# Optimization experiments

Measured on AMD Instinct MI355X. Metric: run time of the kernel, lower is better.

Reference implementation:

```python
import jax, jax.numpy as jnp
import numpy as np

B, S, D, H = 2, 2048, 1024, 16
HD = D // H  # head_size = 64


def setup_inputs() -> dict:
    key = jax.random.key(0)
    ks = jax.random.split(key, 11)
    s = 1.0 / np.sqrt(D)
    inp = {
        "q": jax.random.normal(ks[0], (B, S, D), jnp.float32),
        "k": jax.random.normal(ks[1], (B, S, D), jnp.float32),
        "v": jax.random.normal(ks[2], (B, S, D), jnp.float32),
        "Wq": jax.random.normal(ks[3], (D, D), jnp.float32) * s,
        "bq": jax.random.normal(ks[4], (D,), jnp.float32) * s,
        "Wk": jax.random.normal(ks[5], (D, D), jnp.float32) * s,
        "bk": jax.random.normal(ks[6], (D,), jnp.float32) * s,
        "Wv": jax.random.normal(ks[7], (D, D), jnp.float32) * s,
        "bv": jax.random.normal(ks[8], (D,), jnp.float32) * s,
        "Wo": jax.random.normal(ks[9], (D, D), jnp.float32) * s,
        "bo": jax.random.normal(ks[10], (D,), jnp.float32) * s,
    }
    return inp


def reference(q, k, v, Wq, bq, Wk, bk, Wv, bv, Wo, bo):
    # project and split heads: [B,S,D] -> [B,H,S,HD]
    def split_heads(x, W, b):
        y = x @ W.T + b
        return y.reshape(B, S, H, HD).transpose(0, 2, 1, 3)

    qh = split_heads(q, Wq, bq)
    kh = split_heads(k, Wk, bk)
    vh = split_heads(v, Wv, bv)

    scale = 1.0 / jnp.sqrt(jnp.asarray(HD, qh.dtype))
    scores = jnp.einsum("bhqd,bhkd->bhqk", qh, kh) * scale  # [B,H,S,S]
    weights = jax.nn.softmax(scores, axis=-1)
    out = jnp.einsum("bhqk,bhkd->bhqd", weights, vh)  # [B,H,S,HD]
    out = out.transpose(0, 2, 1, 3).reshape(B, S, D)
    return out @ Wo.T + bo
```

## Files before the change

kernel.cpp:

```cpp
#include <hip/hip_runtime.h>

typedef __attribute__((ext_vector_type(4))) float f32x4;
typedef __attribute__((ext_vector_type(8))) short bf16x8;
typedef __attribute__((ext_vector_type(8))) unsigned short u16x8;
typedef __attribute__((ext_vector_type(4))) unsigned short u16x4;
typedef __attribute__((ext_vector_type(4))) unsigned int u32x4;
typedef unsigned short ushort_t;

#define LOG2E 1.4426950408889634f

__device__ inline unsigned short f2bf(float x) {
  union { float f; unsigned int u; } v; v.f = x;
  unsigned int r = v.u + 0x7fffu + ((v.u >> 16) & 1u);
  return (unsigned short)(r >> 16);
}

__device__ inline unsigned cvtpk_bf16(float a, float b) {
  unsigned r;
  asm("v_cvt_pk_bf16_f32 %0, %1, %2" : "=v"(r) : "v"(a), "v"(b));
  return r;
}

__device__ inline void gload_lds16(const void* g, void* l) {
  __builtin_amdgcn_global_load_lds(
      (const __attribute__((address_space(1))) unsigned int*)g,
      (__attribute__((address_space(3))) unsigned int*)l, 16, 0, 0);
}

__device__ inline void cvt_body(const float* __restrict__ src, ushort_t* __restrict__ dst, int i) {
  const f32x4* s = (const f32x4*)src;
  f32x4 a = s[2 * i], b = s[2 * i + 1];
  u16x8 o;
#pragma unroll
  for (int j = 0; j < 4; ++j) { o[j] = f2bf(a[j]); o[4 + j] = f2bf(b[j]); }
  *(u16x8*)(dst + (size_t)i * 8) = o;
}

__global__ __launch_bounds__(256) void cvt_bf16(const float* __restrict__ src,
                                                ushort_t* __restrict__ dst, int n8) {
  int i = blockIdx.x * 256 + threadIdx.x;
  if (i < n8) cvt_body(src, dst, i);
}

__global__ __launch_bounds__(256) void cvt3(const float* __restrict__ a,
                                            const float* __restrict__ b,
                                            const float* __restrict__ c,
                                            ushort_t* __restrict__ dst, int n8) {
  int i = blockIdx.x * 256 + threadIdx.x;
  if (i >= n8) return;
  const float* s = blockIdx.y == 0 ? a : (blockIdx.y == 1 ? b : c);
  cvt_body(s, dst + (size_t)blockIdx.y * n8 * 8, i);
}

__global__ __launch_bounds__(256) void cvt4(const float* __restrict__ a,
                                            const float* __restrict__ b,
                                            const float* __restrict__ c,
                                            const float* __restrict__ d,
                                            ushort_t* __restrict__ dst, int n8) {
  int i = blockIdx.x * 256 + threadIdx.x;
  if (i >= n8) return;
  const float* s = blockIdx.y == 0 ? a : (blockIdx.y == 1 ? b : (blockIdx.y == 2 ? c : d));
  cvt_body(s, dst + (size_t)blockIdx.y * n8 * 8, i);
}

template <typename F>
__device__ inline void gemm_core(const ushort_t* __restrict__ A, const ushort_t* __restrict__ W,
                                 int m0, int n0, ushort_t* As, ushort_t* Bs, F&& mfma_step) {
  constexpr int K = 1024;
  const int tid = threadIdx.x, lane = tid & 63, wid = tid >> 6;
  const int srow = lane >> 2, sp = lane & 3;
  for (int k0 = 0; k0 < K; k0 += 32) {
#pragma unroll
    for (int c = 0; c < 2; ++c) {
      int i = wid * 2 + c;
      int row = i * 16 + srow;
      int s = sp ^ ((row >> 1) & 3);
      gload_lds16(A + (size_t)(m0 + row) * K + k0 + s * 8, &As[i * 512]);
      gload_lds16(W + (size_t)(n0 + row) * K + k0 + s * 8, &Bs[i * 512]);
    }
    __syncthreads();
    mfma_step(As, Bs);
    __syncthreads();
  }
}

__global__ __launch_bounds__(256) void proj_gemm(const ushort_t* __restrict__ Abase, int aStride,
                                                 const ushort_t* __restrict__ Wall, int wStride,
                                                 const float* __restrict__ bq,
                                                 const float* __restrict__ bk,
                                                 const float* __restrict__ bv, float qs,
                                                 ushort_t* __restrict__ outQ,
                                                 ushort_t* __restrict__ outK,
                                                 ushort_t* __restrict__ outV, int zofs) {
  __shared__ __attribute__((aligned(16))) ushort_t As[128 * 32];
  __shared__ __attribute__((aligned(16))) ushort_t Bs[128 * 32];
  const int z = blockIdx.z + zofs;
  const ushort_t* A = Abase + (size_t)z * aStride;
  const ushort_t* W = Wall + (size_t)z * wStride;
  const float* bias = z == 0 ? bq : (z == 1 ? bk : bv);
  const float scale = z == 0 ? qs : 1.0f;
  ushort_t* out = z == 0 ? outQ : (z == 1 ? outK : outV);
  const int mode = z == 2 ? 1 : 0;

  const int tid = threadIdx.x, lane = tid & 63, wid = tid >> 6;
  const int m0 = blockIdx.x * 128, n0 = blockIdx.y * 128;
  const int wm = wid >> 1, wn = wid & 1;
  const int qr = lane & 15, kq = lane >> 4;
  f32x4 acc[4][4] = {};

  gemm_core(A, W, m0, n0, As, Bs, [&](ushort_t* as, ushort_t* bs) {
    bf16x8 a[4], b[4];
#pragma unroll
    for (int f = 0; f < 4; ++f) {
      int ra = wm * 64 + f * 16 + qr;
      a[f] = *(const bf16x8*)&as[ra * 32 + (kq ^ ((ra >> 1) & 3)) * 8];
      int rb = wn * 64 + f * 16 + qr;
      b[f] = *(const bf16x8*)&bs[rb * 32 + (kq ^ ((rb >> 1) & 3)) * 8];
    }
#pragma unroll
    for (int i = 0; i < 4; ++i)
#pragma unroll
      for (int j = 0; j < 4; ++j)
        acc[i][j] = __builtin_amdgcn_mfma_f32_16x16x32_bf16(a[i], b[j], acc[i][j], 0, 0, 0);
  });

  const int cm = m0 + wm * 64, cn = n0 + wn * 64;
#pragma unroll
  for (int fn = 0; fn < 4; ++fn) {
    int n = cn + fn * 16 + qr;
    float bvv = bias[n];
    int h = n >> 6, hd = n & 63;
#pragma unroll
    for (int fm = 0; fm < 4; ++fm) {
      int m = cm + fm * 16 + kq * 4;
      if (mode == 0) {
#pragma unroll
        for (int r = 0; r < 4; ++r) {
          int mm = m + r, b = mm >> 11, s = mm & 2047;
          out[((size_t)(b * 16 + h) * 2048 + s) * 64 + hd] = f2bf((acc[fm][fn][r] + bvv) * scale);
        }
      } else {
        int b = m >> 11, s = m & 2047;
        u16x4 pk;
#pragma unroll
        for (int r = 0; r < 4; ++r) pk[r] = f2bf((acc[fm][fn][r] + bvv) * scale);
        *(u16x4*)&out[((size_t)(b * 16 + h) * 64 + hd) * 2048 + s] = pk;
      }
    }
  }
}

__global__ __launch_bounds__(256) void gemm_out(const ushort_t* __restrict__ A,
                                                const ushort_t* __restrict__ W,
                                                const float* __restrict__ bias,
                                                float* __restrict__ out) {
  __shared__ __attribute__((aligned(16))) ushort_t As[128 * 32];
  __shared__ __attribute__((aligned(16))) ushort_t Bs[128 * 32];
  const int tid = threadIdx.x, lane = tid & 63, wid = tid >> 6;
  const int m0 = blockIdx.x * 128, n0 = blockIdx.y * 128;
  const int wm = wid >> 1, wn = wid & 1;
  const int qr = lane & 15, kq = lane >> 4;
  f32x4 acc[4][4] = {};

  gemm_core(A, W, m0, n0, As, Bs, [&](ushort_t* as, ushort_t* bs) {
    bf16x8 a[4], b[4];
#pragma unroll
    for (int f = 0; f < 4; ++f) {
      int ra = wm * 64 + f * 16 + qr;
      a[f] = *(const bf16x8*)&as[ra * 32 + (kq ^ ((ra >> 1) & 3)) * 8];
      int rb = wn * 64 + f * 16 + qr;
      b[f] = *(const bf16x8*)&bs[rb * 32 + (kq ^ ((rb >> 1) & 3)) * 8];
    }
#pragma unroll
    for (int i = 0; i < 4; ++i)
#pragma unroll
      for (int j = 0; j < 4; ++j)
        acc[i][j] = __builtin_amdgcn_mfma_f32_16x16x32_bf16(a[i], b[j], acc[i][j], 0, 0, 0);
  });

  const int cm = m0 + wm * 64, cn = n0 + wn * 64;
#pragma unroll
  for (int fn = 0; fn < 4; ++fn) {
    int n = cn + fn * 16 + qr;
    float bvv = bias[n];
#pragma unroll
    for (int fm = 0; fm < 4; ++fm) {
      int m = cm + fm * 16 + kq * 4;
#pragma unroll
      for (int r = 0; r < 4; ++r) out[(size_t)(m + r) * 1024 + n] = acc[fm][fn][r] + bvv;
    }
  }
}

__global__ __launch_bounds__(256) void attn_fwd(const ushort_t* __restrict__ Qh,
                                                const ushort_t* __restrict__ Kh,
                                                const ushort_t* __restrict__ Vt,
                                                ushort_t* __restrict__ ctx) {
  constexpr int S = 2048, HD = 64, NT = S / 64;
  __shared__ __attribute__((aligned(16))) ushort_t Ks[2][64 * 64];
  __shared__ __attribute__((aligned(16))) ushort_t Vs[2][64 * 64];

  const int tid = threadIdx.x, lane = tid & 63, wid = tid >> 6;
  const int bh = blockIdx.y, qt = blockIdx.x;
  const size_t head = (size_t)bh * S * HD;
  const ushort_t* Qp = Qh + head;
  const ushort_t* Kp = Kh + head;
  const ushort_t* Vp = Vt + head;

  const int qr = lane & 15, kq = lane >> 4;
  const int q0 = qt * 128 + wid * 32;

  bf16x8 qfA[2], qfB[2];
#pragma unroll
  for (int kh = 0; kh < 2; ++kh) {
    qfA[kh] = *(const bf16x8*)&Qp[(size_t)(q0 + qr) * HD + kh * 32 + kq * 8];
    qfB[kh] = *(const bf16x8*)&Qp[(size_t)(q0 + 16 + qr) * HD + kh * 32 + kq * 8];
  }

  f32x4 accA[4] = {}, accB[4] = {};
  float mrunA = -3e38f, lrunA = 0.f;
  float mrunB = -3e38f, lrunB = 0.f;

  const int srow8 = lane >> 3, sp8 = lane & 7;

  for (int t = 0; t < NT; ++t) {
    const int buf = t & 1;
    {
      int kv0 = t == 0 ? 0 : (t + 1) * 64;
      int dbuf = t == 0 ? 0 : buf ^ 1;
      if (t == 0 || t + 1 < NT) {
#pragma unroll
        for (int c = 0; c < 2; ++c) {
          int i = wid * 2 + c;
          int row = i * 8 + srow8;
          int s = sp8 ^ (row & 7);
          gload_lds16(&Kp[(size_t)(kv0 + row) * HD + s * 8], &Ks[dbuf][i * 512]);
          gload_lds16(&Vp[(size_t)row * S + kv0 + s * 8], &Vs[dbuf][i * 512]);
        }
      }
      if (t == 0) {
        __syncthreads();
        if (NT > 1) {
#pragma unroll
          for (int c = 0; c < 2; ++c) {
            int i = wid * 2 + c;
            int row = i * 8 + srow8;
            int s = sp8 ^ (row & 7);
            gload_lds16(&Kp[(size_t)(64 + row) * HD + s * 8], &Ks[1][i * 512]);
            gload_lds16(&Vp[(size_t)row * S + 64 + s * 8], &Vs[1][i * 512]);
          }
        }
      }
    }

    f32x4 scA[4] = {}, scB[4] = {};
    __builtin_amdgcn_s_setprio(1);
#pragma unroll
    for (int fn = 0; fn < 4; ++fn) {
      int rk = fn * 16 + qr;
#pragma unroll
      for (int kh = 0; kh < 2; ++kh) {
        bf16x8 kf = *(const bf16x8*)&Ks[buf][rk * 64 + (((kh * 4 + kq) ^ (rk & 7)) * 8)];
        scA[fn] = __builtin_amdgcn_mfma_f32_16x16x32_bf16(kf, qfA[kh], scA[fn], 0, 0, 0);
        scB[fn] = __builtin_amdgcn_mfma_f32_16x16x32_bf16(kf, qfB[kh], scB[fn], 0, 0, 0);
      }
    }
    __builtin_amdgcn_s_setprio(0);

    unsigned wvA[4][2], wvB[4][2];
    {
      float t0 = fmaxf(fmaxf(fmaxf(scA[0][0], scA[0][1]), scA[0][2]), scA[0][3]);
      float t1 = fmaxf(fmaxf(fmaxf(scA[1][0], scA[1][1]), scA[1][2]), scA[1][3]);
      float t2 = fmaxf(fmaxf(fmaxf(scA[2][0], scA[2][1]), scA[2][2]), scA[2][3]);
      float t3 = fmaxf(fmaxf(fmaxf(scA[3][0], scA[3][1]), scA[3][2]), scA[3][3]);
      float pm = fmaxf(fmaxf(t0, t1), fmaxf(t2, t3));
      pm = fmaxf(pm, __shfl_xor(pm, 16, 64));
      pm = fmaxf(pm, __shfl_xor(pm, 32, 64));
      bool need = pm > mrunA + 8.0f;
      if (__any(need)) {
        float mn = need ? pm : mrunA;
        float sf = __builtin_amdgcn_exp2f(mrunA - mn);
        mrunA = mn;
#pragma unroll
        for (int f2 = 0; f2 < 4; ++f2) accA[f2] *= sf;
        lrunA *= sf;
      }
      float sum = 0.f;
#pragma unroll
      for (int fn = 0; fn < 4; ++fn)
#pragma unroll
        for (int r = 0; r < 4; ++r) {
          float p = __builtin_amdgcn_exp2f(scA[fn][r] - mrunA);
          scA[fn][r] = p;
          sum += p;
        }
      sum += __shfl_xor(sum, 16, 64);
      sum += __shfl_xor(sum, 32, 64);
      lrunA += sum;
#pragma unroll
      for (int fn = 0; fn < 4; ++fn) {
        wvA[fn][0] = cvtpk_bf16(scA[fn][0], scA[fn][1]);
        wvA[fn][1] = cvtpk_bf16(scA[fn][2], scA[fn][3]);
      }
    }
    {
      float t0 = fmaxf(fmaxf(fmaxf(scB[0][0], scB[0][1]), scB[0][2]), scB[0][3]);
      float t1 = fmaxf(fmaxf(fmaxf(scB[1][0], scB[1][1]), scB[1][2]), scB[1][3]);
      float t2 = fmaxf(fmaxf(fmaxf(scB[2][0], scB[2][1]), scB[2][2]), scB[2][3]);
      float t3 = fmaxf(fmaxf(fmaxf(scB[3][0], scB[3][1]), scB[3][2]), scB[3][3]);
      float pm = fmaxf(fmaxf(t0, t1), fmaxf(t2, t3));
      pm = fmaxf(pm, __shfl_xor(pm, 16, 64));
      pm = fmaxf(pm, __shfl_xor(pm, 32, 64));
      bool need = pm > mrunB + 8.0f;
      if (__any(need)) {
        float mn = need ? pm : mrunB;
        float sf = __builtin_amdgcn_exp2f(mrunB - mn);
        mrunB = mn;
#pragma unroll
        for (int f2 = 0; f2 < 4; ++f2) accB[f2] *= sf;
        lrunB *= sf;
      }
      float sum = 0.f;
#pragma unroll
      for (int fn = 0; fn < 4; ++fn)
#pragma unroll
        for (int r = 0; r < 4; ++r) {
          float p = __builtin_amdgcn_exp2f(scB[fn][r] - mrunB);
          scB[fn][r] = p;
          sum += p;
        }
      sum += __shfl_xor(sum, 16, 64);
      sum += __shfl_xor(sum, 32, 64);
      lrunB += sum;
#pragma unroll
      for (int fn = 0; fn < 4; ++fn) {
        wvB[fn][0] = cvtpk_bf16(scB[fn][0], scB[fn][1]);
        wvB[fn][1] = cvtpk_bf16(scB[fn][2], scB[fn][3]);
      }
    }

    __builtin_amdgcn_s_setprio(1);
#pragma unroll
    for (int ks = 0; ks < 2; ++ks) {
      unsigned a0 = wvA[2 * ks][0], b0 = wvA[2 * ks + 1][0];
      unsigned a1 = wvA[2 * ks][1], b1 = wvA[2 * ks + 1][1];
      asm volatile("v_permlane32_swap_b32 %0, %1" : "+v"(a0), "+v"(b0));
      asm volatile("v_permlane16_swap_b32 %0, %1" : "+v"(a0), "+v"(b0));
      asm volatile("v_permlane32_swap_b32 %0, %1" : "+v"(a1), "+v"(b1));
      asm volatile("v_permlane16_swap_b32 %0, %1" : "+v"(a1), "+v"(b1));
      u32x4 prawA; prawA[0] = a0; prawA[1] = a1; prawA[2] = b0; prawA[3] = b1;
      bf16x8 pfA = __builtin_bit_cast(bf16x8, prawA);
      unsigned c0 = wvB[2 * ks][0], d0 = wvB[2 * ks + 1][0];
      unsigned c1 = wvB[2 * ks][1], d1 = wvB[2 * ks + 1][1];
      asm volatile("v_permlane32_swap_b32 %0, %1" : "+v"(c0), "+v"(d0));
      asm volatile("v_permlane16_swap_b32 %0, %1" : "+v"(c0), "+v"(d0));
      asm volatile("v_permlane32_swap_b32 %0, %1" : "+v"(c1), "+v"(d1));
      asm volatile("v_permlane16_swap_b32 %0, %1" : "+v"(c1), "+v"(d1));
      u32x4 prawB; prawB[0] = c0; prawB[1] = c1; prawB[2] = d0; prawB[3] = d1;
      bf16x8 pfB = __builtin_bit_cast(bf16x8, prawB);
#pragma unroll
      for (int f2 = 0; f2 < 4; ++f2) {
        int rv = f2 * 16 + qr;
        bf16x8 vf = *(const bf16x8*)&Vs[buf][rv * 64 + (((ks * 4 + kq) ^ (rv & 7)) * 8)];
        accA[f2] = __builtin_amdgcn_mfma_f32_16x16x32_bf16(vf, pfA, accA[f2], 0, 0, 0);
        accB[f2] = __builtin_amdgcn_mfma_f32_16x16x32_bf16(vf, pfB, accB[f2], 0, 0, 0);
      }
    }
    __builtin_amdgcn_s_setprio(0);
    __syncthreads();
  }

  const int b = bh >> 4, h = bh & 15;
  float invA = 1.0f / lrunA, invB = 1.0f / lrunB;
#pragma unroll
  for (int f2 = 0; f2 < 4; ++f2) {
    int col = h * 64 + f2 * 16 + kq * 4;
    u16x4 pkA, pkB;
#pragma unroll
    for (int r = 0; r < 4; ++r) {
      pkA[r] = f2bf(accA[f2][r] * invA);
      pkB[r] = f2bf(accB[f2][r] * invB);
    }
    *(u16x4*)&ctx[((size_t)b * 2048 + q0 + qr) * 1024 + col] = pkA;
    *(u16x4*)&ctx[((size_t)b * 2048 + q0 + 16 + qr) * 1024 + col] = pkB;
  }
}

extern "C" void kernel_launch(void* const* d_in, const int* in_sizes, int n_in,
                              void* d_out, int out_size, void* d_ws, size_t ws_size,
                              hipStream_t stream) {
  const float* q = (const float*)d_in[0];
  const float* k = (const float*)d_in[1];
  const float* v = (const float*)d_in[2];
  const float* Wq = (const float*)d_in[3];
  const float* bq = (const float*)d_in[4];
  const float* Wk = (const float*)d_in[5];
  const float* bk = (const float*)d_in[6];
  const float* Wv = (const float*)d_in[7];
  const float* bv = (const float*)d_in[8];
  const float* Wo = (const float*)d_in[9];
  const float* bo = (const float*)d_in[10];

  char* ws = (char*)d_ws;
  const size_t MB = 1024 * 1024;
  const int NXE = 4194304;
  const int NWE = 1048576;
  const float qs = 0.125f * LOG2E;
  dim3 gg(32, 8), ga(16, 32);

  if (ws_size >= 56 * MB) {
    ushort_t* Xb = (ushort_t*)(ws);
    ushort_t* Wb = (ushort_t*)(ws + 24 * MB);
    ushort_t* Qh = (ushort_t*)(ws + 32 * MB);
    ushort_t* Kh = (ushort_t*)(ws + 40 * MB);
    ushort_t* Vt = (ushort_t*)(ws + 48 * MB);
    cvt3<<<dim3(2048, 3), 256, 0, stream>>>(q, k, v, Xb, NXE / 8);
    cvt4<<<dim3(512, 4), 256, 0, stream>>>(Wq, Wk, Wv, Wo, Wb, NWE / 8);
    proj_gemm<<<dim3(32, 8, 3), 256, 0, stream>>>(Xb, NXE, Wb, NWE, bq, bk, bv, qs,
                                                  Qh, Kh, Vt, 0);
    attn_fwd<<<ga, 256, 0, stream>>>(Qh, Kh, Vt, Xb);
    gemm_out<<<gg, 256, 0, stream>>>(Xb, Wb + (size_t)3 * NWE, bo, (float*)d_out);
  } else if (ws_size >= 40 * MB) {
    ushort_t* Xb = (ushort_t*)(ws);
    ushort_t* Wb = (ushort_t*)(ws + 8 * MB);
    ushort_t* Qh = (ushort_t*)(ws + 16 * MB);
    ushort_t* Kh = (ushort_t*)(ws + 24 * MB);
    ushort_t* Vt = (ushort_t*)(ws + 32 * MB);
    cvt4<<<dim3(512, 4), 256, 0, stream>>>(Wq, Wk, Wv, Wo, Wb, NWE / 8);
    const float* xs[3] = {q, k, v};
    for (int z = 0; z < 3; ++z) {
      cvt_bf16<<<2048, 256, 0, stream>>>(xs[z], Xb, NXE / 8);
      proj_gemm<<<dim3(32, 8, 1), 256, 0, stream>>>(Xb, 0, Wb, NWE, bq, bk, bv, qs,
                                                    Qh, Kh, Vt, z);
    }
    attn_fwd<<<ga, 256, 0, stream>>>(Qh, Kh, Vt, Xb);
    gemm_out<<<gg, 256, 0, stream>>>(Xb, Wb + (size_t)3 * NWE, bo, (float*)d_out);
  } else {
    ushort_t* Xb = (ushort_t*)(ws);
    ushort_t* Wb = (ushort_t*)(ws + 8 * MB);
    ushort_t* Qh = (ushort_t*)(ws + 10 * MB);
    ushort_t* Kh = (ushort_t*)(ws + 18 * MB);
    ushort_t* Vt = (ushort_t*)(ws + 26 * MB);
    const float* xs[3] = {q, k, v};
    const float* wsrc[3] = {Wq, Wk, Wv};
    for (int z = 0; z < 3; ++z) {
      cvt_bf16<<<2048, 256, 0, stream>>>(xs[z], Xb, NXE / 8);
      cvt_bf16<<<512, 256, 0, stream>>>(wsrc[z], Wb, NWE / 8);
      proj_gemm<<<dim3(32, 8, 1), 256, 0, stream>>>(Xb, 0, Wb, 0, bq, bk, bv, qs,
                                                    Qh, Kh, Vt, z);
    }
    attn_fwd<<<ga, 256, 0, stream>>>(Qh, Kh, Vt, Xb);
    cvt_bf16<<<512, 256, 0, stream>>>(Wo, Wb, NWE / 8);
    gemm_out<<<gg, 256, 0, stream>>>(Xb, Wb, bo, (float*)d_out);
  }
}
```

Baseline: 156.6 us.

## Load K/V fragments directly from global memory into registers, dropping LDS staging

The attention kernel no longer stages K and V tiles through double-buffered shared memory with async global-to-LDS loads and block barriers. Each wave now reads its own K and V MFMA fragments straight from global memory into registers every iteration, and the loop is unrolled by two. This removes the __syncthreads barriers and the LDS traffic. In exchange, all four waves in a block redundantly fetch the same K/V tile from global memory/L2, and nothing prefetches ahead, so load latency is exposed.

After: 208.5 us. 33.2% more time.

```diff
diff --git a/kernel.cpp b/kernel.cpp
--- a/kernel.cpp
+++ b/kernel.cpp
@@ -197,9 +197,6 @@
                                                 const ushort_t* __restrict__ Vt,
                                                 ushort_t* __restrict__ ctx) {
   constexpr int S = 2048, HD = 64, NT = S / 64;
-  __shared__ __attribute__((aligned(16))) ushort_t Ks[2][64 * 64];
-  __shared__ __attribute__((aligned(16))) ushort_t Vs[2][64 * 64];
-
   const int tid = threadIdx.x, lane = tid & 63, wid = tid >> 6;
   const int bh = blockIdx.y, qt = blockIdx.x;
   const size_t head = (size_t)bh * S * HD;
@@ -221,48 +218,32 @@
   float mrunA = -3e38f, lrunA = 0.f;
   float mrunB = -3e38f, lrunB = 0.f;
 
-  const int srow8 = lane >> 3, sp8 = lane & 7;
-
+#pragma unroll 2
   for (int t = 0; t < NT; ++t) {
-    const int buf = t & 1;
-    {
-      int kv0 = t == 0 ? 0 : (t + 1) * 64;
-      int dbuf = t == 0 ? 0 : buf ^ 1;
-      if (t == 0 || t + 1 < NT) {
-#pragma unroll
-        for (int c = 0; c < 2; ++c) {
-          int i = wid * 2 + c;
-          int row = i * 8 + srow8;
-          int s = sp8 ^ (row & 7);
-          gload_lds16(&Kp[(size_t)(kv0 + row) * HD + s * 8], &Ks[dbuf][i * 512]);
-          gload_lds16(&Vp[(size_t)row * S + kv0 + s * 8], &Vs[dbuf][i * 512]);
-        }
-      }
-      if (t == 0) {
-        __syncthreads();
-        if (NT > 1) {
-#pragma unroll
-          for (int c = 0; c < 2; ++c) {
-            int i = wid * 2 + c;
-            int row = i * 8 + srow8;
-            int s = sp8 ^ (row & 7);
-            gload_lds16(&Kp[(size_t)(64 + row) * HD + s * 8], &Ks[1][i * 512]);
-            gload_lds16(&Vp[(size_t)row * S + 64 + s * 8], &Vs[1][i * 512]);
-          }
-        }
-      }
-    }
+    const int kv0 = t * 64;
+
+    bf16x8 kf[4][2];
+#pragma unroll
+    for (int fn = 0; fn < 4; ++fn)
+#pragma unroll
+      for (int kh = 0; kh < 2; ++kh)
+        kf[fn][kh] = *(const bf16x8*)&Kp[(size_t)(kv0 + fn * 16 + qr) * HD + kh * 32 + kq * 8];
+
+    bf16x8 vf[2][4];
+#pragma unroll
+    for (int ks = 0; ks < 2; ++ks)
+#pragma unroll
+      for (int f2 = 0; f2 < 4; ++f2)
+        vf[ks][f2] = *(const bf16x8*)&Vp[(size_t)(f2 * 16 + qr) * S + kv0 + ks * 32 + kq * 8];
 
     f32x4 scA[4] = {}, scB[4] = {};
     __builtin_amdgcn_s_setprio(1);
 #pragma unroll
     for (int fn = 0; fn < 4; ++fn) {
-      int rk = fn * 16 + qr;
 #pragma unroll
       for (int kh = 0; kh < 2; ++kh) {
-        bf16x8 kf = *(const bf16x8*)&Ks[buf][rk * 64 + (((kh * 4 + kq) ^ (rk & 7)) * 8)];
-        scA[fn] = __builtin_amdgcn_mfma_f32_16x16x32_bf16(kf, qfA[kh], scA[fn], 0, 0, 0);
-        scB[fn] = __builtin_amdgcn_mfma_f32_16x16x32_bf16(kf, qfB[kh], scB[fn], 0, 0, 0);
+        scA[fn] = __builtin_amdgcn_mfma_f32_16x16x32_bf16(kf[fn][kh], qfA[kh], scA[fn], 0, 0, 0);
+        scB[fn] = __builtin_amdgcn_mfma_f32_16x16x32_bf16(kf[fn][kh], qfB[kh], scB[fn], 0, 0, 0);
       }
     }
     __builtin_amdgcn_s_setprio(0);
@@ -360,14 +341,11 @@
       bf16x8 pfB = __builtin_bit_cast(bf16x8, prawB);
 #pragma unroll
       for (int f2 = 0; f2 < 4; ++f2) {
-        int rv = f2 * 16 + qr;
-        bf16x8 vf = *(const bf16x8*)&Vs[buf][rv * 64 + (((ks * 4 + kq) ^ (rv & 7)) * 8)];
-        accA[f2] = __builtin_amdgcn_mfma_f32_16x16x32_bf16(vf, pfA, accA[f2], 0, 0, 0);
-        accB[f2] = __builtin_amdgcn_mfma_f32_16x16x32_bf16(vf, pfB, accB[f2], 0, 0, 0);
+        accA[f2] = __builtin_amdgcn_mfma_f32_16x16x32_bf16(vf[ks][f2], pfA, accA[f2], 0, 0, 0);
+        accB[f2] = __builtin_amdgcn_mfma_f32_16x16x32_bf16(vf[ks][f2], pfB, accB[f2], 0, 0, 0);
       }
     }
     __builtin_amdgcn_s_setprio(0);
-    __syncthreads();
   }
 
   const int b = bh >> 4, h = bh & 15;
```
